# Optimization experiments

Hardware: AMD Instinct MI355X
Metric: run time of the kernel (lower is better)

The kernel has to match this reference:

```python
import jax, jax.numpy as jnp
import numpy as np

B, L, D, H = 2, 2048, 1024, 16
Dh = D // H


def setup_inputs() -> dict:
    key = jax.random.key(0)
    k = jax.random.split(key, 6)
    s = 1.0 / np.sqrt(D).astype(np.float32)
    return {
        "x": jax.random.normal(k[0], (B, L, D), jnp.float32),
        "mask": jnp.ones((B, L), jnp.int32),
        "user_emb": jax.random.normal(k[1], (B, D), jnp.float32),
        "W_q": jax.random.normal(k[2], (D, D), jnp.float32) * s,
        "W_k": jax.random.normal(k[3], (D, D), jnp.float32) * s,
        "W_v": jax.random.normal(k[4], (D, D), jnp.float32) * s,
        "W_o": jax.random.normal(k[5], (D, D), jnp.float32) * s,
    }


def reference(x, mask, user_emb, W_q, W_k, W_v, W_o):
    b, l, d = x.shape
    # torch nn.Linear(bias=False): y = x @ W.T
    Q = x @ W_q.T
    K = x @ W_k.T
    V = x @ W_v.T

    def split(t):  # [B,L,D] -> [B,H,L,Dh]
        return t.reshape(b, l, H, Dh).transpose(0, 2, 1, 3)

    Qh, Kh, Vh = split(Q), split(K), split(V)

    # additive_bias: rank-1 per-head user bias, [B,H,L,1]
    u = user_emb.reshape(b, H, Dh)
    bias = jnp.einsum('bhld,bhd->bhl', Qh, u)[..., None]

    scores = jnp.einsum('bhld,bhmd->bhlm', Qh, Kh) / np.float32(np.sqrt(Dh))
    scores = scores + bias
    # padding mask: 1 = valid, 0 = pad (broadcast over query dim)
    scores = jnp.where(mask[:, None, None, :] == 0, -jnp.inf, scores)
    # causal mask
    causal = jnp.triu(jnp.ones((l, l), jnp.bool_), k=1)
    scores = jnp.where(causal, -jnp.inf, scores)

    attn = jax.nn.softmax(scores, axis=-1)  # dropout p=0 -> identity
    ctx = jnp.einsum('bhlm,bhmd->bhld', attn, Vh)
    out = ctx.transpose(0, 2, 1, 3).reshape(b, l, d)
    return out @ W_o.T
```

## Files before the change

### kernel.cpp

```cpp
#include <hip/hip_runtime.h>
#include <hip/hip_bf16.h>
#include <stdint.h>

#define Bc 2
#define Lc 2048
#define Dc 1024
#define Hc 16
#define DHc 64

using f32x4  = __attribute__((ext_vector_type(4))) float;
using f32x16 = __attribute__((ext_vector_type(16))) float;
using bf16x8 = __attribute__((ext_vector_type(8))) short;
using bf16x4 = __attribute__((ext_vector_type(4))) short;

static __device__ __forceinline__ unsigned short f2bf(float f) {
  __hip_bfloat16 h = __float2bfloat16(f);
  return __builtin_bit_cast(unsigned short, h);
}
static __device__ __forceinline__ float bf2f(unsigned short u) {
  unsigned int x = ((unsigned int)u) << 16;
  return __builtin_bit_cast(float, x);
}
static __device__ __forceinline__ unsigned int cvtpk(float a, float b) {
  unsigned int r;
  asm("v_cvt_pk_bf16_f32 %0, %1, %2" : "=v"(r) : "v"(a), "v"(b));
  return r;
}

static __device__ __forceinline__ void gload16(const void* g, void* l) {
  __builtin_amdgcn_global_load_lds(
      (const __attribute__((address_space(1))) unsigned int*)g,
      (__attribute__((address_space(3))) unsigned int*)l, 16, 0, 0);
}

__global__ __launch_bounds__(256) void cvt_kernel(
    const float* __restrict__ x,  const float* __restrict__ wq,
    const float* __restrict__ wk, const float* __restrict__ wv,
    const float* __restrict__ wo,
    unsigned short* __restrict__ xb,  unsigned short* __restrict__ wqb,
    unsigned short* __restrict__ wkb, unsigned short* __restrict__ wvb,
    unsigned short* __restrict__ wob) {
  int i = (blockIdx.x * 256 + threadIdx.x) * 4;
  const float* src; unsigned short* dst; int off;
  if (i < 4194304) { src = x; dst = xb; off = i; }
  else {
    int j = i - 4194304; int w = j >> 20; off = j & 1048575;
    src = w == 0 ? wq : w == 1 ? wk : w == 2 ? wv : wo;
    dst = w == 0 ? wqb : w == 1 ? wkb : w == 2 ? wvb : wob;
  }
  float4 v = *(const float4*)(src + off);
  ushort4 u;
  u.x = f2bf(v.x); u.y = f2bf(v.y); u.z = f2bf(v.z); u.w = f2bf(v.w);
  *(ushort4*)(dst + off) = u;
}

template <int MODE>
static __device__ __forceinline__ void gemm_body(
    const unsigned short* __restrict__ A, const unsigned short* __restrict__ Bw,
    void* __restrict__ Cout, float scale, char* lds, int tm, int tn) {
  const int t = threadIdx.x, w = t >> 6, l = t & 63;
  const int wr = w >> 1, wc = w & 1;
  f32x4 zz = {0.f, 0.f, 0.f, 0.f};
  f32x4 acc[4][4];
  for (int a = 0; a < 4; a++)
    for (int b = 0; b < 4; b++) acc[a][b] = zz;
  const char* Ag = (const char*)A;
  const char* Bg = (const char*)Bw;
  const int s0i = w * 64;

  auto stage = [&](int bi, int kt) {
    char* base = lds + bi * 32768;
    const int kb = kt * 128;
#pragma unroll
    for (int i = 0; i < 4; i++) {
      int s = i * 256 + s0i + l;
      int row = s >> 3;
      int c = s & 7;
      int cs = (c ^ (row & 7)) * 16;
      gload16(Ag + (size_t)(tm + row) * 2048 + kb + cs,
              base + (i * 256 + s0i) * 16);
      gload16(Bg + (size_t)(tn + row) * 2048 + kb + cs,
              base + 16384 + (i * 256 + s0i) * 16);
    }
  };

  stage(0, 0);
  for (int kt = 0; kt < 16; ++kt) {
    const int cur = kt & 1;
    const char* Ab = lds + cur * 32768;
    const char* Bb = Ab + 16384;
    if (kt + 1 < 16) {
      stage(cur ^ 1, kt + 1);
      asm volatile("s_waitcnt vmcnt(8)" ::: "memory");
    } else {
      asm volatile("s_waitcnt vmcnt(0)" ::: "memory");
    }
    __builtin_amdgcn_sched_barrier(0);
    __builtin_amdgcn_s_barrier();
    __builtin_amdgcn_sched_barrier(0);

    bf16x8 af[4][2], bfg[4][2];
#pragma unroll
    for (int mm = 0; mm < 4; mm++) {
      int row = wr * 64 + mm * 16 + (l & 15);
      int rsw = (row & 7) << 4;
#pragma unroll
      for (int kk = 0; kk < 2; kk++)
        af[mm][kk] = *(const bf16x8*)(Ab + row * 128 +
                                      ((kk * 64 + (l >> 4) * 16) ^ rsw));
    }
#pragma unroll
    for (int nn = 0; nn < 4; nn++) {
      int row = wc * 64 + nn * 16 + (l & 15);
      int rsw = (row & 7) << 4;
#pragma unroll
      for (int kk = 0; kk < 2; kk++)
        bfg[nn][kk] = *(const bf16x8*)(Bb + row * 128 +
                                       ((kk * 64 + (l >> 4) * 16) ^ rsw));
    }
#pragma unroll
    for (int kk = 0; kk < 2; kk++)
#pragma unroll
      for (int mm = 0; mm < 4; mm++)
#pragma unroll
        for (int nn = 0; nn < 4; nn++)
          acc[mm][nn] = __builtin_amdgcn_mfma_f32_16x16x32_bf16(
              af[mm][kk], bfg[nn][kk], acc[mm][nn], 0, 0, 0);
    __builtin_amdgcn_sched_barrier(0);
    __builtin_amdgcn_s_barrier();
  }

#pragma unroll
  for (int mm = 0; mm < 4; mm++) {
#pragma unroll
    for (int nn = 0; nn < 4; nn++) {
      int col = tn + wc * 64 + nn * 16 + (l & 15);
#pragma unroll
      for (int r = 0; r < 4; r++) {
        int row = tm + wr * 64 + mm * 16 + (l >> 4) * 4 + r;
        if (MODE == 0) {
          int b = row >> 11, ll = row & 2047, h = col >> 6, d = col & 63;
          ((unsigned short*)Cout)[(((b * Hc + h) << 11) + ll) * 64 + d] =
              f2bf(acc[mm][nn][r] * scale);
        } else if (MODE == 1) {
          ((float*)Cout)[row * 1024 + col] = acc[mm][nn][r];
        } else {
          int h = row >> 6, d = row & 63, b = col >> 11, ll = col & 2047;
          ((unsigned short*)Cout)[(((b * Hc + h) * 64 + d) << 11) + ll] =
              f2bf(acc[mm][nn][r]);
        }
      }
    }
  }
}

__global__ __launch_bounds__(256) void gemm_qkv(
    const unsigned short* __restrict__ xb,
    const unsigned short* __restrict__ wq, const unsigned short* __restrict__ wk,
    const unsigned short* __restrict__ wv,
    unsigned short* __restrict__ q, unsigned short* __restrict__ k,
    unsigned short* __restrict__ vT) {
  __shared__ char lds[65536];
  int z = blockIdx.z;
  if (z < 2) {
    gemm_body<0>(xb, z == 0 ? wq : wk, z == 0 ? q : k,
                 z == 0 ? 0.125f * 1.44269504089f : 1.0f,
                 lds, blockIdx.x * 128, blockIdx.y * 128);
  } else {
    gemm_body<2>(wv, xb, vT, 1.0f, lds, blockIdx.y * 128, blockIdx.x * 128);
  }
}

__global__ __launch_bounds__(256) void gemm_out(
    const unsigned short* __restrict__ ctx, const unsigned short* __restrict__ wo,
    float* __restrict__ out) {
  __shared__ char lds[65536];
  gemm_body<1>(ctx, wo, out, 1.0f, lds, blockIdx.x * 128, blockIdx.y * 128);
}

__device__ const int g_qt[36]  = {7,6,5,15,15,15,15,14,14,11,11,11,10,4,13,13,13,13,14,14,12,12,10,10,9,9,3,12,12,9,8,8,8,2,1,0};
__device__ const int g_kb0[36] = {0,0,0,0,8,16,24,0,8,0,8,16,0,0,0,7,14,21,16,23,0,7,8,15,0,7,0,14,20,14,0,6,12,0,0,0};
__device__ const int g_kb1[36] = {16,14,12,8,16,24,32,8,16,8,16,24,8,10,7,14,21,28,23,30,7,14,15,22,7,14,8,20,26,20,6,12,18,6,4,2};
__device__ const int g_pid[36] = {-1,-1,-1,0,1,2,3,4,5,16,17,18,19,-1,8,9,10,11,6,7,12,13,20,21,22,23,-1,14,15,24,25,26,27,-1,-1,-1};

__global__ __launch_bounds__(256, 4) void attn_kernel(
    const unsigned short* __restrict__ Q, const unsigned short* __restrict__ Kg,
    const unsigned short* __restrict__ VT,
    unsigned short* __restrict__ Op, float2* __restrict__ ml,
    unsigned short* __restrict__ ctx) {
  __shared__ char lds[32768];
  const int t = threadIdx.x, w = t >> 6, l = t & 63;
  const int hi = l >> 5, q32 = l & 31;
  const int idx = blockIdx.x;
  const int bh = idx & 31;
  const int g = idx >> 5;
  const int qt  = g_qt[g];
  const int kb0 = g_kb0[g];
  const int kb1 = g_kb1[g];
  const int pid = g_pid[g];
  const unsigned short* Qb = Q + bh * (Lc * DHc);
  const unsigned short* Kb = Kg + bh * (Lc * DHc);
  const unsigned short* Vb = VT + bh * (Lc * DHc);
  const int qrow = qt * 128 + w * 32 + q32;

  bf16x8 qf[4];
#pragma unroll
  for (int s = 0; s < 4; s++)
    qf[s] = *(const bf16x8*)(Qb + qrow * 64 + s * 16 + hi * 8);

  const f32x16 z16 = {0.f,0.f,0.f,0.f,0.f,0.f,0.f,0.f,
                      0.f,0.f,0.f,0.f,0.f,0.f,0.f,0.f};
  float mi = -1e30f, li = 0.f;
  f32x16 accO[2];
  accO[0] = z16; accO[1] = z16;

  const int s0i = w * 64 + l;
  auto stage = [&](int bi, int kb) {
    char* Ksb = lds + bi * 8192;
    char* Vsb = lds + 16384 + bi * 8192;
#pragma unroll
    for (int i = 0; i < 2; i++) {
      int s = i * 256 + s0i;
      int row = s >> 3;
      int cb = ((s & 7) * 16) ^ ((row & 7) << 4);
      gload16((const char*)Kb + (kb * 64 + row) * 128 + cb,
              Ksb + (i * 256 + w * 64) * 16);
      gload16((const char*)Vb + row * 4096 + kb * 128 + cb,
              Vsb + (i * 256 + w * 64) * 16);
    }
  };

  stage(0, kb0);
  for (int kb = kb0; kb < kb1; ++kb) {
    const int cur = (kb - kb0) & 1;
    char* Ks = lds + cur * 8192;
    char* Vs = lds + 16384 + cur * 8192;
    if (kb + 1 < kb1) {
      stage(cur ^ 1, kb + 1);
      asm volatile("s_waitcnt vmcnt(4)" ::: "memory");
    } else {
      asm volatile("s_waitcnt vmcnt(0)" ::: "memory");
    }
    __builtin_amdgcn_sched_barrier(0);
    __builtin_amdgcn_s_barrier();
    __builtin_amdgcn_sched_barrier(0);

    f32x16 sf[2];
    sf[0] = z16; sf[1] = z16;
    __builtin_amdgcn_s_setprio(1);
#pragma unroll
    for (int blk = 0; blk < 2; blk++) {
      int row = blk * 32 + q32;
      int rsw = (row & 7) << 4;
#pragma unroll
      for (int s = 0; s < 4; s++) {
        bf16x8 kf = *(const bf16x8*)(Ks + row * 128 + (((2 * s + hi) * 16) ^ rsw));
        sf[blk] = __builtin_amdgcn_mfma_f32_32x32x16_bf16(kf, qf[s], sf[blk], 0, 0, 0);
      }
    }
    __builtin_amdgcn_s_setprio(0);

    if (kb * 64 + 63 > qt * 128 + w * 32) {
#pragma unroll
      for (int blk = 0; blk < 2; blk++)
#pragma unroll
        for (int r = 0; r < 16; r++) {
          int kg = kb * 64 + blk * 32 + (r & 3) + 8 * (r >> 2) + 4 * hi;
          if (kg > qrow) sf[blk][r] = -1e30f;
        }
    }

    float tm16[16];
#pragma unroll
    for (int r = 0; r < 16; r++) tm16[r] = fmaxf(sf[0][r], sf[1][r]);
#pragma unroll
    for (int r = 0; r < 8; r++) tm16[r] = fmaxf(tm16[r], tm16[r + 8]);
#pragma unroll
    for (int r = 0; r < 4; r++) tm16[r] = fmaxf(tm16[r], tm16[r + 4]);
    float pm = fmaxf(fmaxf(tm16[0], tm16[1]), fmaxf(tm16[2], tm16[3]));
    pm = fmaxf(pm, __shfl_xor(pm, 32));

    if (!__all(pm - mi <= 8.f)) {
      float corr = __builtin_amdgcn_exp2f(mi - pm);
      mi = pm;
      li *= corr;
#pragma unroll
      for (int db = 0; db < 2; db++)
#pragma unroll
        for (int r = 0; r < 16; r++) accO[db][r] *= corr;
    }

    float a16[16];
#pragma unroll
    for (int r = 0; r < 16; r++) {
      float p0 = __builtin_amdgcn_exp2f(sf[0][r] - mi);
      float p1 = __builtin_amdgcn_exp2f(sf[1][r] - mi);
      sf[0][r] = p0; sf[1][r] = p1;
      a16[r] = p0 + p1;
    }
#pragma unroll
    for (int r = 0; r < 8; r++) a16[r] += a16[r + 8];
#pragma unroll
    for (int r = 0; r < 4; r++) a16[r] += a16[r + 4];
    float rs = (a16[0] + a16[1]) + (a16[2] + a16[3]);
    rs += __shfl_xor(rs, 32);
    li += rs;

    bf16x8 pf[4];
#pragma unroll
    for (int kw = 0; kw < 4; kw++) {
      const int bkl = kw >> 1, o = (kw & 1) * 8;
      unsigned int a01 = cvtpk(sf[bkl][o + 0], sf[bkl][o + 1]);
      unsigned int a23 = cvtpk(sf[bkl][o + 2], sf[bkl][o + 3]);
      unsigned int b01 = cvtpk(sf[bkl][o + 4], sf[bkl][o + 5]);
      unsigned int b23 = cvtpk(sf[bkl][o + 6], sf[bkl][o + 7]);
      auto s1 = __builtin_amdgcn_permlane32_swap(a01, b01, false, false);
      auto s2 = __builtin_amdgcn_permlane32_swap(a23, b23, false, false);
      uint4 uu;
      uu.x = s1[0];
      uu.y = s2[0];
      uu.z = s1[1];
      uu.w = s2[1];
      pf[kw] = __builtin_bit_cast(bf16x8, uu);
    }

    __builtin_amdgcn_s_setprio(1);
#pragma unroll
    for (int kw = 0; kw < 4; kw++) {
#pragma unroll
      for (int db = 0; db < 2; db++) {
        int row = db * 32 + q32;
        int rsw = (row & 7) << 4;
        bf16x8 vf = *(const bf16x8*)(Vs + row * 128 + (((2 * kw + hi) * 16) ^ rsw));
        accO[db] = __builtin_amdgcn_mfma_f32_32x32x16_bf16(vf, pf[kw], accO[db], 0, 0, 0);
      }
    }
    __builtin_amdgcn_s_setprio(0);
    __builtin_amdgcn_sched_barrier(0);
    __builtin_amdgcn_s_barrier();
  }

  const int b = bh >> 4, h = bh & 15;
  if (pid < 0) {
    float inv = 1.0f / li;
    unsigned short* dst = ctx + (size_t)(b * Lc + qrow) * Dc + h * 64;
#pragma unroll
    for (int db = 0; db < 2; db++)
#pragma unroll
      for (int rq = 0; rq < 4; rq++) {
        int d0 = db * 32 + 8 * rq + 4 * hi;
        bf16x4 v4;
#pragma unroll
        for (int j = 0; j < 4; j++) v4[j] = (short)f2bf(accO[db][rq * 4 + j] * inv);
        *(bf16x4*)(dst + d0) = v4;
      }
  } else {
    unsigned short* Opc = Op + (size_t)(bh * 28 + pid) * 8192;
    const int ql = w * 32 + q32;
#pragma unroll
    for (int db = 0; db < 2; db++)
#pragma unroll
      for (int rq = 0; rq < 4; rq++) {
        int d0 = db * 32 + 8 * rq + 4 * hi;
        bf16x4 v4;
#pragma unroll
        for (int j = 0; j < 4; j++) v4[j] = (short)f2bf(accO[db][rq * 4 + j]);
        *(bf16x4*)(Opc + ql * 64 + d0) = v4;
      }
    if (hi == 0) ml[(bh * 28 + pid) * 128 + ql] = make_float2(mi, li);
  }
}

__device__ const int c_pb[8]  = {25, 22, 19, 16, 12, 8, 4, 0};
__device__ const int c_nch[8] = { 3,  3,  3,  3,  4, 4, 4, 4};

__global__ __launch_bounds__(256) void combine_kernel(
    const unsigned short* __restrict__ Op, const float2* __restrict__ ml,
    unsigned short* __restrict__ ctx) {
  const int cb = blockIdx.x;
  const int qq = cb >> 5, bh = cb & 31;
  const int qt = 8 + qq;
  const int pb = c_pb[qq], nch = c_nch[qq];
  const int t = threadIdx.x;
  const int ql = t >> 1, dh = (t & 1) * 32;
  float2 pp[4];
  float mx = -1e30f;
#pragma unroll
  for (int j = 0; j < 4; j++) {
    int jj = j < nch ? j : 0;
    float2 v = ml[(size_t)(bh * 28 + pb + jj) * 128 + ql];
    pp[j] = (j < nch) ? v : make_float2(-1e30f, 0.f);
    mx = fmaxf(mx, pp[j].x);
  }
  float wgt[4];
  float den = 0.f;
#pragma unroll
  for (int j = 0; j < 4; j++) {
    float e = __builtin_amdgcn_exp2f(pp[j].x - mx);
    den += pp[j].y * e;
    wgt[j] = e;
  }
  float inv = 1.0f / den;
#pragma unroll
  for (int j = 0; j < 4; j++) wgt[j] *= inv;
  const int b = bh >> 4, h = bh & 15;
  unsigned short* dst = ctx + (size_t)(b * Lc + qt * 128 + ql) * Dc + h * 64 + dh;
#pragma unroll
  for (int seg = 0; seg < 4; seg++) {
    float a8[8] = {0.f, 0.f, 0.f, 0.f, 0.f, 0.f, 0.f, 0.f};
#pragma unroll
    for (int j = 0; j < 4; j++) {
      int jj = j < nch ? j : 0;
      bf16x8 o = *(const bf16x8*)(Op + (size_t)(bh * 28 + pb + jj) * 8192 +
                                  ql * 64 + dh + seg * 8);
#pragma unroll
      for (int e = 0; e < 8; e++) a8[e] += wgt[j] * bf2f((unsigned short)o[e]);
    }
    bf16x8 outv;
#pragma unroll
    for (int e = 0; e < 8; e++) outv[e] = (short)f2bf(a8[e]);
    *(bf16x8*)(dst + seg * 8) = outv;
  }
}

extern "C" void kernel_launch(void* const* d_in, const int* in_sizes, int n_in,
                              void* d_out, int out_size, void* d_ws, size_t ws_size,
                              hipStream_t stream) {
  const float* x  = (const float*)d_in[0];
  const float* Wq = (const float*)d_in[3];
  const float* Wk = (const float*)d_in[4];
  const float* Wv = (const float*)d_in[5];
  const float* Wo = (const float*)d_in[6];

  char* ws = (char*)d_ws;
  const size_t MB = 1024 * 1024;
  unsigned short* xb  = (unsigned short*)(ws);
  unsigned short* wqb = (unsigned short*)(ws + 8 * MB);
  unsigned short* wkb = (unsigned short*)(ws + 10 * MB);
  unsigned short* wvb = (unsigned short*)(ws + 12 * MB);
  unsigned short* q   = (unsigned short*)(ws + 16 * MB);
  unsigned short* k   = (unsigned short*)(ws + 24 * MB);
  unsigned short* vT  = (unsigned short*)(ws + 32 * MB);
  unsigned short* ctx = (unsigned short*)(ws + 40 * MB);
  unsigned short* wob = (unsigned short*)(ws + 48 * MB);
  unsigned short* Op  = (unsigned short*)(ws);
  float2*         ml  = (float2*)(ws + 50 * MB);

  cvt_kernel<<<8192, 256, 0, stream>>>(x, Wq, Wk, Wv, Wo, xb, wqb, wkb, wvb, wob);
  gemm_qkv<<<dim3(32, 8, 3), 256, 0, stream>>>(xb, wqb, wkb, wvb, q, k, vT);
  attn_kernel<<<1152, 256, 0, stream>>>(q, k, vT, Op, ml, ctx);
  combine_kernel<<<256, 256, 0, stream>>>(Op, ml, ctx);
  gemm_out<<<dim3(32, 8, 1), 256, 0, stream>>>(ctx, wob, (float*)d_out);
}
```

Baseline: 99.48 us.

## Rewrite QKV projection GEMM with 256x256 tiles and interleaved prefetch

Replaces the 128x128 templated QKV GEMM with a dedicated 512-thread kernel using 256x256 output tiles, 128KB LDS double buffering, and global-load prefetches split across four MFMA phases with priority hints. All three projections are computed as W·x^T so Q/K stores become vectorized 4-wide writes along head dim. The aim is more data reuse per tile and better overlap of loads with matrix math. The cost is a grid of only 192 blocks, which may underfill the GPU's compute units, plus high register and LDS use. gemm_out is inlined from the template unchanged, and combine gets a small address hoist.

New measurement: 101.1 us. About the same (+1.6%).

```diff
diff --git a/kernel.cpp b/kernel.cpp
--- a/kernel.cpp
+++ b/kernel.cpp
@@ -54,18 +54,193 @@
   *(ushort4*)(dst + off) = u;
 }
 
-template <int MODE>
-static __device__ __forceinline__ void gemm_body(
-    const unsigned short* __restrict__ A, const unsigned short* __restrict__ Bw,
-    void* __restrict__ Cout, float scale, char* lds, int tm, int tn) {
+__global__ __launch_bounds__(512) void gemm_qkv256(
+    const unsigned short* __restrict__ xb,
+    const unsigned short* __restrict__ wq, const unsigned short* __restrict__ wk,
+    const unsigned short* __restrict__ wv,
+    unsigned short* __restrict__ q, unsigned short* __restrict__ k,
+    unsigned short* __restrict__ vT) {
+  __shared__ char lds[131072];
+  const int t = threadIdx.x;
+  const int wid = t >> 6, l = t & 63;
+  const int wr = wid >> 2, wc = wid & 3;
+  const int tn0 = blockIdx.x * 256;
+  const int my = blockIdx.y;
+  const int wsel = my >> 2;
+  const int tm = (my & 3) * 256;
+  const unsigned short* W = wsel == 0 ? wq : wsel == 1 ? wk : wv;
+
+  f32x4 zz = {0.f, 0.f, 0.f, 0.f};
+  f32x4 acc[8][4];
+#pragma unroll
+  for (int a = 0; a < 8; a++)
+#pragma unroll
+    for (int b = 0; b < 4; b++) acc[a][b] = zz;
+
+  const int rin = t >> 3;
+  const int coff = (((t & 7) ^ (rin & 7)) << 4);
+  const char* Asrc0 = (const char*)W + (size_t)(tm + rin) * 2048 + coff;
+  const char* Bsrc0 = (const char*)xb + (size_t)(tn0 + rin) * 2048 + coff;
+
+#define STG_A(bi, kt1, g)                                                     \
+  gload16(Asrc0 + (size_t)(g) * 131072 + (kt1) * 128,                         \
+          lds + (bi) * 65536 + (g) * 8192 + wid * 1024)
+#define STG_B(bi, kt1, g)                                                     \
+  gload16(Bsrc0 + (size_t)(g) * 131072 + (kt1) * 128,                         \
+          lds + (bi) * 65536 + 32768 + (g) * 8192 + wid * 1024)
+
+  STG_A(0, 0, 0); STG_A(0, 0, 2);
+  STG_B(0, 0, 0); STG_B(0, 0, 1);
+  STG_B(0, 0, 2); STG_B(0, 0, 3);
+  STG_A(0, 0, 1); STG_A(0, 0, 3);
+
+  const int cA = (l >> 4);
+  const int rsw = l & 7;
+
+  for (int kt = 0; kt < 16; ++kt) {
+    const int cur = kt & 1;
+    const char* Ab = lds + cur * 65536;
+    const char* Bb = Ab + 32768;
+    const int nxt = cur ^ 1;
+    const bool pre = (kt + 1 < 16);
+    const int k1 = kt + 1;
+    bf16x8 bfr[4];
+
+    asm volatile("s_waitcnt vmcnt(2)" ::: "memory");
+    __builtin_amdgcn_sched_barrier(0);
+    __builtin_amdgcn_s_barrier();
+    __builtin_amdgcn_sched_barrier(0);
+#pragma unroll
+    for (int nn = 0; nn < 4; nn++) {
+      int rb = wc * 64 + nn * 16 + (l & 15);
+      bfr[nn] = *(const bf16x8*)(Bb + rb * 128 + ((cA ^ rsw) << 4));
+    }
+    {
+      bf16x8 afr[4];
+#pragma unroll
+      for (int mm = 0; mm < 4; mm++) {
+        int ra = wr * 128 + mm * 16 + (l & 15);
+        afr[mm] = *(const bf16x8*)(Ab + ra * 128 + ((cA ^ rsw) << 4));
+      }
+      if (pre) { STG_A(nxt, k1, 0); STG_A(nxt, k1, 2); }
+      __builtin_amdgcn_s_setprio(1);
+#pragma unroll
+      for (int mm = 0; mm < 4; mm++)
+#pragma unroll
+        for (int nn = 0; nn < 4; nn++)
+          acc[mm][nn] = __builtin_amdgcn_mfma_f32_16x16x32_bf16(
+              afr[mm], bfr[nn], acc[mm][nn], 0, 0, 0);
+      __builtin_amdgcn_s_setprio(0);
+    }
+
+    if (pre) {
+      asm volatile("s_waitcnt vmcnt(2)" ::: "memory");
+    } else {
+      asm volatile("s_waitcnt vmcnt(0)" ::: "memory");
+    }
+    __builtin_amdgcn_sched_barrier(0);
+    __builtin_amdgcn_s_barrier();
+    __builtin_amdgcn_sched_barrier(0);
+    {
+      bf16x8 afr[4];
+#pragma unroll
+      for (int mm = 0; mm < 4; mm++) {
+        int ra = wr * 128 + 64 + mm * 16 + (l & 15);
+        afr[mm] = *(const bf16x8*)(Ab + ra * 128 + ((cA ^ rsw) << 4));
+      }
+      if (pre) { STG_B(nxt, k1, 0); STG_B(nxt, k1, 1); }
+      __builtin_amdgcn_s_setprio(1);
+#pragma unroll
+      for (int mm = 0; mm < 4; mm++)
+#pragma unroll
+        for (int nn = 0; nn < 4; nn++)
+          acc[4 + mm][nn] = __builtin_amdgcn_mfma_f32_16x16x32_bf16(
+              afr[mm], bfr[nn], acc[4 + mm][nn], 0, 0, 0);
+      __builtin_amdgcn_s_setprio(0);
+    }
+
+#pragma unroll
+    for (int nn = 0; nn < 4; nn++) {
+      int rb = wc * 64 + nn * 16 + (l & 15);
+      bfr[nn] = *(const bf16x8*)(Bb + rb * 128 + (((4 + cA) ^ rsw) << 4));
+    }
+    {
+      bf16x8 afr[4];
+#pragma unroll
+      for (int mm = 0; mm < 4; mm++) {
+        int ra = wr * 128 + mm * 16 + (l & 15);
+        afr[mm] = *(const bf16x8*)(Ab + ra * 128 + (((4 + cA) ^ rsw) << 4));
+      }
+      if (pre) { STG_B(nxt, k1, 2); STG_B(nxt, k1, 3); }
+      __builtin_amdgcn_s_setprio(1);
+#pragma unroll
+      for (int mm = 0; mm < 4; mm++)
+#pragma unroll
+        for (int nn = 0; nn < 4; nn++)
+          acc[mm][nn] = __builtin_amdgcn_mfma_f32_16x16x32_bf16(
+              afr[mm], bfr[nn], acc[mm][nn], 0, 0, 0);
+      __builtin_amdgcn_s_setprio(0);
+    }
+
+    {
+      bf16x8 afr[4];
+#pragma unroll
+      for (int mm = 0; mm < 4; mm++) {
+        int ra = wr * 128 + 64 + mm * 16 + (l & 15);
+        afr[mm] = *(const bf16x8*)(Ab + ra * 128 + (((4 + cA) ^ rsw) << 4));
+      }
+      if (pre) { STG_A(nxt, k1, 1); STG_A(nxt, k1, 3); }
+      __builtin_amdgcn_s_setprio(1);
+#pragma unroll
+      for (int mm = 0; mm < 4; mm++)
+#pragma unroll
+        for (int nn = 0; nn < 4; nn++)
+          acc[4 + mm][nn] = __builtin_amdgcn_mfma_f32_16x16x32_bf16(
+              afr[mm], bfr[nn], acc[4 + mm][nn], 0, 0, 0);
+      __builtin_amdgcn_s_setprio(0);
+    }
+  }
+#undef STG_A
+#undef STG_B
+
+  const float scale = (wsel == 0) ? 0.125f * 1.44269504089f : 1.0f;
+#pragma unroll
+  for (int mm8 = 0; mm8 < 8; mm8++) {
+    int f0 = tm + wr * 128 + mm8 * 16 + (l >> 4) * 4;
+    int h = f0 >> 6, d0 = f0 & 63;
+#pragma unroll
+    for (int nn = 0; nn < 4; nn++) {
+      int col = tn0 + wc * 64 + nn * 16 + (l & 15);
+      int b = col >> 11, ll = col & 2047;
+      if (wsel < 2) {
+        bf16x4 v4;
+#pragma unroll
+        for (int r = 0; r < 4; r++) v4[r] = (short)f2bf(acc[mm8][nn][r] * scale);
+        unsigned short* dst = wsel == 0 ? q : k;
+        *(bf16x4*)&dst[((((size_t)(b * Hc + h) << 11) + ll) << 6) + d0] = v4;
+      } else {
+#pragma unroll
+        for (int r = 0; r < 4; r++)
+          vT[(((size_t)(b * Hc + h) * 64 + d0 + r) << 11) + ll] =
+              f2bf(acc[mm8][nn][r]);
+      }
+    }
+  }
+}
+
+__global__ __launch_bounds__(256) void gemm_out(
+    const unsigned short* __restrict__ ctx, const unsigned short* __restrict__ wo,
+    float* __restrict__ out) {
+  __shared__ char lds[65536];
   const int t = threadIdx.x, w = t >> 6, l = t & 63;
   const int wr = w >> 1, wc = w & 1;
+  const int tm = blockIdx.x * 128, tn = blockIdx.y * 128;
   f32x4 zz = {0.f, 0.f, 0.f, 0.f};
   f32x4 acc[4][4];
   for (int a = 0; a < 4; a++)
     for (int b = 0; b < 4; b++) acc[a][b] = zz;
-  const char* Ag = (const char*)A;
-  const char* Bg = (const char*)Bw;
+  const char* Ag = (const char*)ctx;
+  const char* Bg = (const char*)wo;
   const int s0i = w * 64;
 
   auto stage = [&](int bi, int kt) {
@@ -75,8 +250,7 @@
     for (int i = 0; i < 4; i++) {
       int s = i * 256 + s0i + l;
       int row = s >> 3;
-      int c = s & 7;
-      int cs = (c ^ (row & 7)) * 16;
+      int cs = (((s & 7) ^ (row & 7))) * 16;
       gload16(Ag + (size_t)(tm + row) * 2048 + kb + cs,
               base + (i * 256 + s0i) * 16);
       gload16(Bg + (size_t)(tn + row) * 2048 + kb + cs,
@@ -138,44 +312,10 @@
 #pragma unroll
       for (int r = 0; r < 4; r++) {
         int row = tm + wr * 64 + mm * 16 + (l >> 4) * 4 + r;
-        if (MODE == 0) {
-          int b = row >> 11, ll = row & 2047, h = col >> 6, d = col & 63;
-          ((unsigned short*)Cout)[(((b * Hc + h) << 11) + ll) * 64 + d] =
-              f2bf(acc[mm][nn][r] * scale);
-        } else if (MODE == 1) {
-          ((float*)Cout)[row * 1024 + col] = acc[mm][nn][r];
-        } else {
-          int h = row >> 6, d = row & 63, b = col >> 11, ll = col & 2047;
-          ((unsigned short*)Cout)[(((b * Hc + h) * 64 + d) << 11) + ll] =
-              f2bf(acc[mm][nn][r]);
-        }
-      }
-    }
-  }
-}
-
-__global__ __launch_bounds__(256) void gemm_qkv(
-    const unsigned short* __restrict__ xb,
-    const unsigned short* __restrict__ wq, const unsigned short* __restrict__ wk,
-    const unsigned short* __restrict__ wv,
-    unsigned short* __restrict__ q, unsigned short* __restrict__ k,
-    unsigned short* __restrict__ vT) {
-  __shared__ char lds[65536];
-  int z = blockIdx.z;
-  if (z < 2) {
-    gemm_body<0>(xb, z == 0 ? wq : wk, z == 0 ? q : k,
-                 z == 0 ? 0.125f * 1.44269504089f : 1.0f,
-                 lds, blockIdx.x * 128, blockIdx.y * 128);
-  } else {
-    gemm_body<2>(wv, xb, vT, 1.0f, lds, blockIdx.y * 128, blockIdx.x * 128);
-  }
-}
-
-__global__ __launch_bounds__(256) void gemm_out(
-    const unsigned short* __restrict__ ctx, const unsigned short* __restrict__ wo,
-    float* __restrict__ out) {
-  __shared__ char lds[65536];
-  gemm_body<1>(ctx, wo, out, 1.0f, lds, blockIdx.x * 128, blockIdx.y * 128);
+        out[(size_t)row * 1024 + col] = acc[mm][nn][r];
+      }
+    }
+  }
 }
 
 __device__ const int g_qt[36]  = {7,6,5,15,15,15,15,14,14,11,11,11,10,4,13,13,13,13,14,14,12,12,10,10,9,9,3,12,12,9,8,8,8,2,1,0};
@@ -405,14 +545,14 @@
   for (int j = 0; j < 4; j++) wgt[j] *= inv;
   const int b = bh >> 4, h = bh & 15;
   unsigned short* dst = ctx + (size_t)(b * Lc + qt * 128 + ql) * Dc + h * 64 + dh;
+  const unsigned short* q0 = Op + (size_t)(bh * 28 + pb) * 8192 + ql * 64 + dh;
 #pragma unroll
   for (int seg = 0; seg < 4; seg++) {
     float a8[8] = {0.f, 0.f, 0.f, 0.f, 0.f, 0.f, 0.f, 0.f};
 #pragma unroll
     for (int j = 0; j < 4; j++) {
       int jj = j < nch ? j : 0;
-      bf16x8 o = *(const bf16x8*)(Op + (size_t)(bh * 28 + pb + jj) * 8192 +
-                                  ql * 64 + dh + seg * 8);
+      bf16x8 o = *(const bf16x8*)(q0 + (size_t)jj * 8192 + seg * 8);
 #pragma unroll
       for (int e = 0; e < 8; e++) a8[e] += wgt[j] * bf2f((unsigned short)o[e]);
     }
@@ -447,8 +587,8 @@
   float2*         ml  = (float2*)(ws + 50 * MB);
 
   cvt_kernel<<<8192, 256, 0, stream>>>(x, Wq, Wk, Wv, Wo, xb, wqb, wkb, wvb, wob);
-  gemm_qkv<<<dim3(32, 8, 3), 256, 0, stream>>>(xb, wqb, wkb, wvb, q, k, vT);
+  gemm_qkv256<<<dim3(16, 12), 512, 0, stream>>>(xb, wqb, wkb, wvb, q, k, vT);
   attn_kernel<<<1152, 256, 0, stream>>>(q, k, vT, Op, ml, ctx);
   combine_kernel<<<256, 256, 0, stream>>>(Op, ml, ctx);
-  gemm_out<<<dim3(32, 8, 1), 256, 0, stream>>>(ctx, wob, (float*)d_out);
-}
+  gemm_out<<<dim3(32, 8), 256, 0, stream>>>(ctx, wob, (float*)d_out);
+}
```
